# Kernel optimization log

Measured on AMD Instinct MI355X. Metric: run time of the kernel, lower is better.

## Reference

```python
import jax, jax.numpy as jnp
import numpy as np

K = 2          # diffusion steps
HID = 64       # hidden_dim
T_OUT = 12     # decoder horizon
EPS = 1e-6


def _random_walk(A):
    # W_fwd = D_out^{-1} A ; W_bwd = D_in^{-1} A^T  (row-normalized)
    W_fwd = A / (A.sum(axis=1, keepdims=True) + EPS)
    AT = A.T
    W_bwd = AT / (AT.sum(axis=1, keepdims=True) + EPS)
    return W_fwd, W_bwd


def _dconv(xin, Wf, Wb, W, b):
    # xin: (B, N, F). K forward + K backward random-walk hops, concat, linear.
    outs = [xin]
    xf = xin
    for _ in range(K):
        xf = jnp.einsum('ij,bjf->bif', Wf, xf)
        outs.append(xf)
    xb = xin
    for _ in range(K):
        xb = jnp.einsum('ij,bjf->bif', Wb, xb)
        outs.append(xb)
    return jnp.concatenate(outs, axis=-1) @ W + b


def _cell(xl, h, Wr, br, Wz, bz, Wn, bn, Wf, Wb):
    xh = jnp.concatenate([xl, h], axis=-1)
    r = jax.nn.sigmoid(_dconv(xh, Wf, Wb, Wr, br))
    z = jax.nn.sigmoid(_dconv(xh, Wf, Wb, Wz, bz))
    xrh = jnp.concatenate([xl, r * h], axis=-1)
    n = jnp.tanh(_dconv(xrh, Wf, Wb, Wn, bn))
    return (1.0 - z) * h + z * n


def setup_inputs() -> dict:
    key = jax.random.key(0)
    ks = jax.random.split(key, 20)
    B, T_in, N = 16, 12, 512
    x = jax.random.normal(ks[0], (B, T_in, N), dtype=jnp.float32)
    A = jax.random.uniform(ks[1], (N, N), dtype=jnp.float32)

    def lin(k, fan_in, fan_out):
        s = 1.0 / np.sqrt(fan_in)
        kw, kb = jax.random.split(k)
        W = jax.random.uniform(kw, (fan_in, fan_out), jnp.float32, -s, s)
        b = jax.random.uniform(kb, (fan_out,), jnp.float32, -s, s)
        return W, b

    in0 = (2 * K + 1) * (1 + HID)    # 325
    in1 = (2 * K + 1) * (2 * HID)    # 640
    Wr0, br0 = lin(ks[2], in0, HID)
    Wz0, bz0 = lin(ks[3], in0, HID)
    Wn0, bn0 = lin(ks[4], in0, HID)
    Wr1, br1 = lin(ks[5], in1, HID)
    Wz1, bz1 = lin(ks[6], in1, HID)
    Wn1, bn1 = lin(ks[7], in1, HID)
    Wp, bp = lin(ks[8], HID, 1)
    return dict(x=x, A=A, Wr0=Wr0, br0=br0, Wz0=Wz0, bz0=bz0, Wn0=Wn0, bn0=bn0,
                Wr1=Wr1, br1=br1, Wz1=Wz1, bz1=bz1, Wn1=Wn1, bn1=bn1, Wp=Wp, bp=bp)


def reference(x, A, Wr0, br0, Wz0, bz0, Wn0, bn0,
              Wr1, br1, Wz1, bz1, Wn1, bn1, Wp, bp):
    Wf, Wb = _random_walk(A)
    B, T_in, N = x.shape
    x4 = x[..., None]                             # (B, T_in, N, 1)
    h0 = jnp.zeros((B, N, HID), x.dtype)
    h1 = jnp.zeros((B, N, HID), x.dtype)

    def enc_step(carry, xt):
        h0, h1 = carry
        h0 = _cell(xt, h0, Wr0, br0, Wz0, bz0, Wn0, bn0, Wf, Wb)
        h1 = _cell(h0, h1, Wr1, br1, Wz1, bz1, Wn1, bn1, Wf, Wb)
        return (h0, h1), None

    (h0, h1), _ = jax.lax.scan(enc_step, (h0, h1), jnp.moveaxis(x4, 1, 0))

    def dec_step(carry, _):
        h0, h1, di = carry
        h0 = _cell(di, h0, Wr0, br0, Wz0, bz0, Wn0, bn0, Wf, Wb)
        h1 = _cell(h0, h1, Wr1, br1, Wz1, bz1, Wn1, bn1, Wf, Wb)
        yt = h1 @ Wp + bp                          # (B, N, 1)
        return (h0, h1, yt), yt

    (_, _, _), ys = jax.lax.scan(dec_step, (h0, h1, x4[:, -1]), None, length=T_OUT)
    return jnp.moveaxis(ys, 0, 1)[..., 0]          # (B, T_out, N)
```

## Files before the change

### kernel.cpp

```cpp
#include <hip/hip_runtime.h>
#include <math.h>

#define T_IN   12
#define T_OUT  12
#define NB     8192
#define EPSV   1e-6f

typedef __attribute__((ext_vector_type(8))) short short8;
typedef __attribute__((ext_vector_type(4))) float floatx4;

__device__ __forceinline__ unsigned short f2bf(float x) {
    union { float f; unsigned u; } v; v.f = x;
    unsigned r = v.u + 0x7fffu + ((v.u >> 16) & 1u);
    return (unsigned short)(r >> 16);
}
__device__ __forceinline__ float bf2f(unsigned short h) {
    union { float f; unsigned u; } v; v.u = ((unsigned)h) << 16;
    return v.f;
}
__device__ __forceinline__ unsigned packbf(float v) {
    unsigned u = __float_as_uint(v);
    unsigned hu = u & 0xffff0000u;
    float r = v - __uint_as_float(hu);
    unsigned ru = __float_as_uint(r);
    return (ru & 0xffff0000u) | (u >> 16);
}

__device__ __forceinline__ float sigmoid_fast(float x) {
    return 1.0f / (1.0f + __expf(-x));
}
__device__ __forceinline__ float tanh_fast(float x) {
    float e = __expf(2.0f * x);
    return 1.0f - 2.0f / (e + 1.0f);
}

struct HopA {
    const float* M[4];
    float* dst0[4];
};

struct HopM {
    const unsigned short* Ahi[4]; const unsigned short* Alo[4];
    const unsigned* src0; const unsigned* src1;
    unsigned* dst0[4]; unsigned* dst1[4];
    int tiles0;
};

struct XHopAll { const float* M[4]; const float* xenc; float* dst; };
struct XHopOne { const float* M[4]; const float* xv; float* dst; };

struct WPack { const float* w[4]; unsigned short* hi[4]; unsigned short* lo[4]; };

struct LPack {
    const float* W; unsigned short* hi; unsigned short* lo;
    int base[10]; int nseg;
};

struct LinA {
    const unsigned* seg[10]; int nseg;
    const float* sx[5]; int sxrow[5]; int nsx;
};

__global__ void sums_kernel(const float* __restrict__ A, float* __restrict__ rs,
                            float* __restrict__ cs) {
    int i = blockIdx.x;
    int t = threadIdx.x;
    __shared__ float s1[256], s2[256];
    float a = A[i * 512 + t] + A[i * 512 + t + 256];
    float b = A[t * 512 + i] + A[(t + 256) * 512 + i];
    s1[t] = a; s2[t] = b;
    __syncthreads();
    for (int off = 128; off > 0; off >>= 1) {
        if (t < off) { s1[t] += s1[t + off]; s2[t] += s2[t + off]; }
        __syncthreads();
    }
    if (t == 0) { rs[i] = s1[0]; cs[i] = s2[0]; }
}

__global__ void fill_kernel(const float* __restrict__ A, const float* __restrict__ rs,
                            const float* __restrict__ cs, float* __restrict__ Wf,
                            float* __restrict__ Wb) {
    int i = blockIdx.x;
    float irs = 1.0f / (rs[i] + EPSV);
    float ics = 1.0f / (cs[i] + EPSV);
    for (int j = threadIdx.x; j < 512; j += 256) {
        Wf[i * 512 + j] = A[i * 512 + j] * irs;
        Wb[i * 512 + j] = A[j * 512 + i] * ics;
    }
}

__global__ void xenc_kernel(const float* __restrict__ x, float* __restrict__ xenc) {
    int idx = blockIdx.x * 256 + threadIdx.x;
    if (idx >= T_IN * NB) return;
    int j = idx & 511;
    int b = (idx >> 9) & 15;
    int t = idx >> 13;
    xenc[t * NB + j * 16 + b] = x[(b * T_IN + t) * 512 + j];
}

__global__ __launch_bounds__(256) void ghop_kernel(HopA a) {
    int z = blockIdx.z;
    const float* Wm = a.M[z];
    const float* X = Wm;
    float* Y = a.dst0[z];
    int col0 = blockIdx.x * 64;
    int row0 = blockIdx.y * 64;
    int tid = threadIdx.x;
    int tx = tid & 15, ty = tid >> 4;
    int kkA = tid & 15, rrA = tid >> 4;
    int ccB = tid & 63, kkB = tid >> 6;

    __shared__ float As[16][68], Bs[16][68];
    float acc[4][4] = {};

    const float* wp = Wm + (row0 + rrA) * 512 + kkA;
    const float* xp = X + (size_t)(col0 + ccB) + (size_t)kkB * 512;

    float ra[4], rb[4];
#pragma unroll
    for (int p = 0; p < 4; ++p) ra[p] = wp[p * 16 * 512];
#pragma unroll
    for (int p = 0; p < 4; ++p) rb[p] = xp[(size_t)(p * 4) * 512];

    for (int k0 = 0; k0 < 512; k0 += 16) {
#pragma unroll
        for (int p = 0; p < 4; ++p) As[kkA][rrA + p * 16] = ra[p];
#pragma unroll
        for (int p = 0; p < 4; ++p) Bs[kkB + p * 4][ccB] = rb[p];
        __syncthreads();
        if (k0 + 16 < 512) {
            int kn = k0 + 16;
#pragma unroll
            for (int p = 0; p < 4; ++p) ra[p] = wp[p * 16 * 512 + kn];
#pragma unroll
            for (int p = 0; p < 4; ++p) rb[p] = xp[(size_t)(kn + p * 4) * 512];
        }
#pragma unroll
        for (int k = 0; k < 16; ++k) {
            const float4 a4 = *(const float4*)&As[k][ty * 4];
            const float4 b4 = *(const float4*)&Bs[k][tx * 4];
            float av[4] = { a4.x, a4.y, a4.z, a4.w };
            float bv[4] = { b4.x, b4.y, b4.z, b4.w };
#pragma unroll
            for (int i = 0; i < 4; ++i)
#pragma unroll
                for (int j = 0; j < 4; ++j)
                    acc[i][j] = fmaf(av[i], bv[j], acc[i][j]);
        }
        __syncthreads();
    }

    int colw = col0 + tx * 4;
#pragma unroll
    for (int i = 0; i < 4; ++i) {
        int row = row0 + ty * 4 + i;
        *(float4*)&Y[(size_t)row * 512 + colw] =
            make_float4(acc[i][0], acc[i][1], acc[i][2], acc[i][3]);
    }
}

__global__ void wpack_kernel(WPack a) {
    int z = blockIdx.y;
    int idx = blockIdx.x * 256 + threadIdx.x;
    int m = idx >> 9, k = idx & 511;
    float x = a.w[z][idx];
    unsigned short h = f2bf(x);
    unsigned short l = f2bf(x - bf2f(h));
    int p = (((m >> 4) * 64 + (k >> 3)) * 16 + (m & 15)) * 8 + (k & 7);
    a.hi[z][p] = h;
    a.lo[z][p] = l;
}

__global__ void lpack_kernel(LPack p) {
    int idx = blockIdx.x * 256 + threadIdx.x;
    if (idx >= p.nseg * 4096) return;
    int j = idx & 7, ln = (idx >> 3) & 15, ntl = (idx >> 7) & 3, O = idx >> 9;
    int s = O >> 3, o8 = O & 7;
    int row = p.base[s] + o8 * 8 + j;
    int col = ntl * 16 + ln;
    float v = p.W[(size_t)row * 64 + col];
    unsigned short h = f2bf(v);
    p.hi[idx] = h;
    p.lo[idx] = f2bf(v - bf2f(h));
}

__global__ void xhop_all_kernel(XHopAll a) {
    int t = blockIdx.z, mz = blockIdx.y;
    int m = blockIdx.x * 16 + (threadIdx.x >> 4);
    int c = threadIdx.x & 15;
    const float* wrow = a.M[mz] + (size_t)m * 512;
    const float* xv = a.xenc + (size_t)t * NB;
    float s[8] = {};
    for (int k = 0; k < 512; k += 8) {
        float4 w0 = *(const float4*)&wrow[k];
        float4 w1 = *(const float4*)&wrow[k + 4];
        s[0] = fmaf(w0.x, xv[(k + 0) * 16 + c], s[0]);
        s[1] = fmaf(w0.y, xv[(k + 1) * 16 + c], s[1]);
        s[2] = fmaf(w0.z, xv[(k + 2) * 16 + c], s[2]);
        s[3] = fmaf(w0.w, xv[(k + 3) * 16 + c], s[3]);
        s[4] = fmaf(w1.x, xv[(k + 4) * 16 + c], s[4]);
        s[5] = fmaf(w1.y, xv[(k + 5) * 16 + c], s[5]);
        s[6] = fmaf(w1.z, xv[(k + 6) * 16 + c], s[6]);
        s[7] = fmaf(w1.w, xv[(k + 7) * 16 + c], s[7]);
    }
    float r = ((s[0] + s[1]) + (s[2] + s[3])) + ((s[4] + s[5]) + (s[6] + s[7]));
    a.dst[((size_t)t * 4 + mz) * NB + m * 16 + c] = r;
}

__global__ void xhop_one_kernel(XHopOne a) {
    int mz = blockIdx.y;
    int m = blockIdx.x * 16 + (threadIdx.x >> 4);
    int c = threadIdx.x & 15;
    const float* wrow = a.M[mz] + (size_t)m * 512;
    const float* xv = a.xv;
    float s[8] = {};
    for (int k = 0; k < 512; k += 8) {
        float4 w0 = *(const float4*)&wrow[k];
        float4 w1 = *(const float4*)&wrow[k + 4];
        s[0] = fmaf(w0.x, xv[(k + 0) * 16 + c], s[0]);
        s[1] = fmaf(w0.y, xv[(k + 1) * 16 + c], s[1]);
        s[2] = fmaf(w0.z, xv[(k + 2) * 16 + c], s[2]);
        s[3] = fmaf(w0.w, xv[(k + 3) * 16 + c], s[3]);
        s[4] = fmaf(w1.x, xv[(k + 4) * 16 + c], s[4]);
        s[5] = fmaf(w1.y, xv[(k + 5) * 16 + c], s[5]);
        s[6] = fmaf(w1.z, xv[(k + 6) * 16 + c], s[6]);
        s[7] = fmaf(w1.w, xv[(k + 7) * 16 + c], s[7]);
    }
    float r = ((s[0] + s[1]) + (s[2] + s[3])) + ((s[4] + s[5]) + (s[6] + s[7]));
    a.dst[(size_t)mz * NB + m * 16 + c] = r;
}

template<int MI>
__global__ __launch_bounds__(256) void hop_mfma(HopM a) {
    int z = blockIdx.z;
    int nt = blockIdx.x;
    const unsigned* X; unsigned* Y; int c0;
    if (nt < a.tiles0) { X = a.src0; Y = a.dst0[z]; c0 = nt * 64; }
    else { X = a.src1; Y = a.dst1[z]; c0 = (nt - a.tiles0) * 64; }
    const unsigned short* Ahi = a.Ahi[z];
    const unsigned short* Alo = a.Alo[z];
    int bm = blockIdx.y * (MI * 32);

    __shared__ unsigned short Bhi_s[2][64][40];
    __shared__ unsigned short Blo_s[2][64][40];

    int tid = threadIdx.x;
    int lane = tid & 63, w = tid >> 6;
    int wm = (w & 1) * (MI * 16), wn = (w >> 1) * 32;
    int ln = lane & 15, quad = lane >> 4;
    int sc = tid & 63, skh = tid >> 6;

    floatx4 acc[MI][2];
#pragma unroll
    for (int mi = 0; mi < MI; ++mi)
#pragma unroll
        for (int ci = 0; ci < 2; ++ci) acc[mi][ci] = (floatx4)0.0f;

    const unsigned* xbase = X + c0 + sc;
    int mtb = (bm + wm) >> 4;

    unsigned uv[8];
#pragma unroll
    for (int j = 0; j < 8; ++j)
        uv[j] = xbase[(size_t)(skh * 8 + j) * 1024];
    {
        short8 h8, l8;
#pragma unroll
        for (int j = 0; j < 8; ++j) {
            h8[j] = (short)(uv[j] & 0xffffu);
            l8[j] = (short)(uv[j] >> 16);
        }
        *(short8*)&Bhi_s[0][sc][skh * 8] = h8;
        *(short8*)&Blo_s[0][sc][skh * 8] = l8;
    }
#pragma unroll
    for (int j = 0; j < 8; ++j)
        uv[j] = xbase[(size_t)(32 + skh * 8 + j) * 1024];

    for (int it = 0; it < 16; ++it) {
        __syncthreads();
        int cur = it & 1;
        if (it + 1 < 16) {
            short8 h8, l8;
#pragma unroll
            for (int j = 0; j < 8; ++j) {
                h8[j] = (short)(uv[j] & 0xffffu);
                l8[j] = (short)(uv[j] >> 16);
            }
            *(short8*)&Bhi_s[cur ^ 1][sc][skh * 8] = h8;
            *(short8*)&Blo_s[cur ^ 1][sc][skh * 8] = l8;
        }
        if (it + 2 < 16) {
            int kn = (it + 2) * 32;
#pragma unroll
            for (int j = 0; j < 8; ++j)
                uv[j] = xbase[(size_t)(kn + skh * 8 + j) * 1024];
        }
        short8 bh[2], bl[2];
#pragma unroll
        for (int ci = 0; ci < 2; ++ci) {
            bh[ci] = *(const short8*)&Bhi_s[cur][wn + ci * 16 + ln][quad * 8];
            bl[ci] = *(const short8*)&Blo_s[cur][wn + ci * 16 + ln][quad * 8];
        }
        int kob = it * 4 + quad;
#pragma unroll
        for (int mi = 0; mi < MI; ++mi) {
            size_t aoff = ((size_t)((mtb + mi) * 64 + kob) * 16 + ln) * 8;
            short8 Ah = *(const short8*)(Ahi + aoff);
            short8 Al = *(const short8*)(Alo + aoff);
#pragma unroll
            for (int ci = 0; ci < 2; ++ci) {
                acc[mi][ci] = __builtin_amdgcn_mfma_f32_16x16x32_bf16(Ah, bh[ci], acc[mi][ci], 0, 0, 0);
                acc[mi][ci] = __builtin_amdgcn_mfma_f32_16x16x32_bf16(Ah, bl[ci], acc[mi][ci], 0, 0, 0);
                acc[mi][ci] = __builtin_amdgcn_mfma_f32_16x16x32_bf16(Al, bh[ci], acc[mi][ci], 0, 0, 0);
            }
        }
    }

#pragma unroll
    for (int mi = 0; mi < MI; ++mi) {
#pragma unroll
        for (int ci = 0; ci < 2; ++ci) {
            int mrow = bm + wm + mi * 16 + quad * 4;
            int col = c0 + wn + ci * 16 + ln;
#pragma unroll
            for (int r = 0; r < 4; ++r)
                Y[(size_t)(mrow + r) * 1024 + col] = packbf(acc[mi][ci][r]);
        }
    }
}

__device__ __forceinline__ void lin_core2(const LinA& a,
        const unsigned short* __restrict__ Bh, const unsigned short* __restrict__ Bl,
        int row0, int ln, int quad, int cihalf, floatx4 acc[2]) {
    for (int s = 0; s < a.nseg; ++s) {
        const unsigned* ap = a.seg[s] + (size_t)(row0 + ln) * 64 + quad * 8;
#pragma unroll
        for (int hh = 0; hh < 2; ++hh) {
            unsigned u[8];
            *(uint4*)&u[0] = *(const uint4*)(ap + hh * 32);
            *(uint4*)&u[4] = *(const uint4*)(ap + hh * 32 + 4);
            short8 Ah, Al;
#pragma unroll
            for (int j = 0; j < 8; ++j) {
                Ah[j] = (short)(u[j] & 0xffffu);
                Al[j] = (short)(u[j] >> 16);
            }
            int O = s * 8 + hh * 4 + quad;
#pragma unroll
            for (int ci = 0; ci < 2; ++ci) {
                int c_abs = cihalf * 2 + ci;
                size_t boff = ((size_t)(O * 4 + c_abs) * 16 + ln) * 8;
                short8 B1 = *(const short8*)(Bh + boff);
                short8 B2 = *(const short8*)(Bl + boff);
                acc[ci] = __builtin_amdgcn_mfma_f32_16x16x32_bf16(Ah, B1, acc[ci], 0, 0, 0);
                acc[ci] = __builtin_amdgcn_mfma_f32_16x16x32_bf16(Al, B1, acc[ci], 0, 0, 0);
                acc[ci] = __builtin_amdgcn_mfma_f32_16x16x32_bf16(Ah, B2, acc[ci], 0, 0, 0);
            }
        }
    }
}

__device__ __forceinline__ void lin_scalar2(const LinA& a, const float* __restrict__ WO,
        int row0, int ln, int quad, int cihalf, floatx4 acc[2]) {
    for (int t = 0; t < a.nsx; ++t) {
        const float* wr = WO + (size_t)a.sxrow[t] * 64;
        const float* sv = a.sx[t] + row0 + quad * 4;
#pragma unroll
        for (int rr = 0; rr < 4; ++rr) {
            float v = sv[rr];
#pragma unroll
            for (int ci = 0; ci < 2; ++ci)
                acc[ci][rr] = fmaf(v, wr[(cihalf * 2 + ci) * 16 + ln], acc[ci][rr]);
        }
    }
}

__global__ __launch_bounds__(256) void lin_rz_mfma(
    LinA a,
    const unsigned short* Wrh, const unsigned short* Wrl, const float* WrO, const float* br,
    const unsigned short* Wzh, const unsigned short* Wzl, const float* WzO, const float* bz,
    const float* __restrict__ h, unsigned* __restrict__ GP, float* __restrict__ Z) {
    int w = threadIdx.x >> 6, lane = threadIdx.x & 63;
    int ln = lane & 15, quad = lane >> 4;
    int row0 = blockIdx.x * 64 + w * 16;
    int gate = blockIdx.y;
    int cihalf = blockIdx.z;
    const unsigned short* Bh = gate ? Wzh : Wrh;
    const unsigned short* Bl = gate ? Wzl : Wrl;
    const float* WO = gate ? WzO : WrO;
    const float* bias = gate ? bz : br;
    floatx4 acc[2];
    acc[0] = (floatx4)0.0f; acc[1] = (floatx4)0.0f;
    lin_core2(a, Bh, Bl, row0, ln, quad, cihalf, acc);
    if (a.nsx) lin_scalar2(a, WO, row0, ln, quad, cihalf, acc);
#pragma unroll
    for (int ci = 0; ci < 2; ++ci) {
        int col = (cihalf * 2 + ci) * 16 + ln;
        float bv = bias[col];
#pragma unroll
        for (int rr = 0; rr < 4; ++rr) {
            int row = row0 + quad * 4 + rr;
            size_t idx = (size_t)row * 64 + col;
            float sg = sigmoid_fast(acc[ci][rr] + bv);
            if (gate == 0) GP[idx] = packbf(sg * h[idx]);
            else Z[idx] = sg;
        }
    }
}

__global__ __launch_bounds__(256) void lin_n_mfma(
    LinA a, const unsigned short* Wnh, const unsigned short* Wnl,
    const float* WnO, const float* bn,
    const float* __restrict__ Zb, float* __restrict__ h, unsigned* __restrict__ hP,
    int doProj, const float* __restrict__ Wp, const float* __restrict__ bp,
    float* __restrict__ out, float* __restrict__ di, int t) {
    int w = threadIdx.x >> 6, lane = threadIdx.x & 63;
    int ln = lane & 15, quad = lane >> 4;
    int cihalf = w & 1, rsub = w >> 1;
    int row0 = (blockIdx.x * 2 + rsub) * 16;
    __shared__ float pr[2][2][16];
    floatx4 acc[2];
    acc[0] = (floatx4)0.0f; acc[1] = (floatx4)0.0f;
    lin_core2(a, Wnh, Wnl, row0, ln, quad, cihalf, acc);
    if (a.nsx) lin_scalar2(a, WnO, row0, ln, quad, cihalf, acc);
    float p[4] = {0.0f, 0.0f, 0.0f, 0.0f};
#pragma unroll
    for (int ci = 0; ci < 2; ++ci) {
        int col = (cihalf * 2 + ci) * 16 + ln;
        float bv = bn[col];
        float wpv = doProj ? Wp[col] : 0.0f;
#pragma unroll
        for (int rr = 0; rr < 4; ++rr) {
            int row = row0 + quad * 4 + rr;
            size_t idx = (size_t)row * 64 + col;
            float nn = tanh_fast(acc[ci][rr] + bv);
            float z = Zb[idx];
            float hv = h[idx];
            float o = (1.0f - z) * hv + z * nn;
            h[idx] = o;
            hP[idx] = packbf(o);
            p[rr] = fmaf(o, wpv, p[rr]);
        }
    }
    if (doProj) {
#pragma unroll
        for (int rr = 0; rr < 4; ++rr) {
            p[rr] += __shfl_xor(p[rr], 1, 64);
            p[rr] += __shfl_xor(p[rr], 2, 64);
            p[rr] += __shfl_xor(p[rr], 4, 64);
            p[rr] += __shfl_xor(p[rr], 8, 64);
        }
        if (ln == 0) {
#pragma unroll
            for (int rr = 0; rr < 4; ++rr)
                pr[cihalf][rsub][quad * 4 + rr] = p[rr];
        }
        __syncthreads();
        if (cihalf == 0 && ln == 0) {
            float bpv = bp[0];
#pragma unroll
            for (int rr = 0; rr < 4; ++rr) {
                int qr = quad * 4 + rr;
                int row = row0 + qr;
                float y = pr[0][rsub][qr] + pr[1][rsub][qr] + bpv;
                int n = row >> 4, b = row & 15;
                out[(b * T_OUT + t) * 512 + n] = y;
                di[row] = y;
            }
        }
    }
}

extern "C" void kernel_launch(void* const* d_in, const int* in_sizes, int n_in,
                              void* d_out, int out_size, void* d_ws, size_t ws_size,
                              hipStream_t stream) {
    (void)in_sizes; (void)n_in; (void)out_size; (void)ws_size;
    const float* x   = (const float*)d_in[0];
    const float* A   = (const float*)d_in[1];
    const float* Wr0 = (const float*)d_in[2];  const float* br0 = (const float*)d_in[3];
    const float* Wz0 = (const float*)d_in[4];  const float* bz0 = (const float*)d_in[5];
    const float* Wn0 = (const float*)d_in[6];  const float* bn0 = (const float*)d_in[7];
    const float* Wr1 = (const float*)d_in[8];  const float* br1 = (const float*)d_in[9];
    const float* Wz1 = (const float*)d_in[10]; const float* bz1 = (const float*)d_in[11];
    const float* Wn1 = (const float*)d_in[12]; const float* bn1 = (const float*)d_in[13];
    const float* Wp  = (const float*)d_in[14]; const float* bp  = (const float*)d_in[15];
    float* out = (float*)d_out;

    float* ws = (float*)d_ws;
    size_t off = 0;
    auto alloc = [&](size_t nf) { float* p = ws + off; off += nf; return p; };
    float* Wf  = alloc(262144); float* Wb  = alloc(262144);
    float* W2f = alloc(262144); float* W2b = alloc(262144);
    float* rs  = alloc(512);    float* cs  = alloc(512);
    float* xenc = alloc((size_t)T_IN * NB);
    unsigned short* Whi[4]; unsigned short* Wlo[4];
    for (int m = 0; m < 4; ++m) Whi[m] = (unsigned short*)alloc(131072);
    for (int m = 0; m < 4; ++m) Wlo[m] = (unsigned short*)alloc(131072);
    unsigned* HAall = (unsigned*)alloc(4 * 524288);
    unsigned* HA_P[4]; for (int m = 0; m < 4; ++m) HA_P[m] = HAall + (size_t)m * 524288;
    unsigned* HB_P[4]; unsigned* HG_P[4];
    for (int m = 0; m < 4; ++m) HB_P[m] = (unsigned*)alloc(524288);
    for (int m = 0; m < 4; ++m) HG_P[m] = (unsigned*)alloc(524288);
    unsigned* GP  = (unsigned*)alloc(524288);
    unsigned* h0P = (unsigned*)alloc(524288);
    unsigned* h1P = (unsigned*)alloc(524288);
    float* Z  = alloc(524288);
    float* h0 = alloc(524288);
    float* h1 = alloc(524288);
    float* XHE = alloc((size_t)T_IN * 4 * NB);
    float* HXSdec = alloc(4 * NB);
    float* di = alloc(NB);
    unsigned short* LWh[6]; unsigned short* LWl[6];
    for (int g = 0; g < 3; ++g) { LWh[g] = (unsigned short*)alloc(10240); LWl[g] = (unsigned short*)alloc(10240); }
    for (int g = 3; g < 6; ++g) { LWh[g] = (unsigned short*)alloc(20480); LWl[g] = (unsigned short*)alloc(20480); }

    hipMemsetAsync(h0, 0, 524288 * sizeof(float), stream);
    hipMemsetAsync(h1, 0, 524288 * sizeof(float), stream);
    hipMemsetAsync(h0P, 0, 524288 * sizeof(unsigned), stream);
    hipMemsetAsync(h1P, 0, 524288 * sizeof(unsigned), stream);
    hipMemsetAsync(HAall, 0, 4ul * 524288 * sizeof(unsigned), stream);

    xenc_kernel<<<dim3((T_IN * NB) / 256), 256, 0, stream>>>(x, xenc);
    sums_kernel<<<dim3(512), 256, 0, stream>>>(A, rs, cs);
    fill_kernel<<<dim3(512), 256, 0, stream>>>(A, rs, cs, Wf, Wb);

    {
        HopA w2 = {};
        w2.M[0] = Wf; w2.M[1] = Wb;
        w2.dst0[0] = W2f; w2.dst0[1] = W2b;
        ghop_kernel<<<dim3(8, 8, 2), 256, 0, stream>>>(w2);
    }
    {
        WPack p;
        p.w[0] = Wf; p.w[1] = W2f; p.w[2] = Wb; p.w[3] = W2b;
        for (int m = 0; m < 4; ++m) { p.hi[m] = Whi[m]; p.lo[m] = Wlo[m]; }
        wpack_kernel<<<dim3(1024, 4), 256, 0, stream>>>(p);
    }
    {
        const float* WG[6] = { Wr0, Wz0, Wn0, Wr1, Wz1, Wn1 };
        for (int g = 0; g < 6; ++g) {
            LPack p = {};
            p.W = WG[g]; p.hi = LWh[g]; p.lo = LWl[g];
            if (g < 3) { p.nseg = 5;  for (int s = 0; s < 5; ++s)  p.base[s] = 65 * s + 1; }
            else       { p.nseg = 10; for (int s = 0; s < 10; ++s) p.base[s] = 64 * s; }
            lpack_kernel<<<dim3((p.nseg * 4096 + 255) / 256), 256, 0, stream>>>(p);
        }
    }
    {
        XHopAll xa;
        xa.M[0] = Wf; xa.M[1] = W2f; xa.M[2] = Wb; xa.M[3] = W2b;
        xa.xenc = xenc; xa.dst = XHE;
        xhop_all_kernel<<<dim3(32, 4, T_IN), 256, 0, stream>>>(xa);
    }

    auto hopcom = [&](HopM& a) {
        for (int m = 0; m < 4; ++m) { a.Ahi[m] = Whi[m]; a.Alo[m] = Wlo[m]; }
    };

    for (int t = 0; t < T_IN + T_OUT; ++t) {
        int dec = (t >= T_IN);
        int td = t - T_IN;
        const float* xcur; const float* hxs;
        if (!dec) { xcur = xenc + (size_t)t * NB; hxs = XHE + (size_t)t * 4 * NB; }
        else if (td == 0) { xcur = xenc + (size_t)(T_IN - 1) * NB; hxs = XHE + (size_t)(T_IN - 1) * 4 * NB; }
        else {
            xcur = di; hxs = HXSdec;
            XHopOne xo;
            xo.M[0] = Wf; xo.M[1] = W2f; xo.M[2] = Wb; xo.M[3] = W2b;
            xo.xv = di; xo.dst = HXSdec;
            xhop_one_kernel<<<dim3(32, 4), 256, 0, stream>>>(xo);
        }

        LinA la = {};
        la.nseg = 5;
        la.seg[0] = h0P;
        for (int m = 0; m < 4; ++m) la.seg[1 + m] = HA_P[m];
        la.nsx = 5;
        la.sx[0] = xcur; la.sxrow[0] = 0;
        for (int m = 0; m < 4; ++m) { la.sx[1 + m] = hxs + (size_t)m * NB; la.sxrow[1 + m] = 65 * (m + 1); }
        lin_rz_mfma<<<dim3(128, 2, 2), 256, 0, stream>>>(la, LWh[0], LWl[0], Wr0, br0,
                                                         LWh[1], LWl[1], Wz0, bz0, h0, GP, Z);
        {
            HopM a = {}; hopcom(a);
            a.src0 = GP; a.tiles0 = 16;
            for (int m = 0; m < 4; ++m) a.dst0[m] = HG_P[m];
            hop_mfma<2><<<dim3(16, 8, 4), 256, 0, stream>>>(a);
        }
        LinA lb = la;
        lb.seg[0] = GP;
        for (int m = 0; m < 4; ++m) lb.seg[1 + m] = HG_P[m];
        lin_n_mfma<<<dim3(256), 256, 0, stream>>>(lb, LWh[2], LWl[2], Wn0, bn0, Z, h0, h0P,
                                                  0, (const float*)nullptr, (const float*)nullptr,
                                                  (float*)nullptr, (float*)nullptr, 0);

        {
            HopM a = {}; hopcom(a);
            a.src0 = h0P; a.tiles0 = 16;
            a.src1 = h1P;
            for (int m = 0; m < 4; ++m) { a.dst0[m] = HA_P[m]; a.dst1[m] = HB_P[m]; }
            hop_mfma<4><<<dim3(32, 4, 4), 256, 0, stream>>>(a);
        }
        LinA lc = {};
        lc.nseg = 10; lc.nsx = 0;
        lc.seg[0] = h0P; lc.seg[1] = h1P;
        for (int m = 0; m < 4; ++m) { lc.seg[2 + 2 * m] = HA_P[m]; lc.seg[3 + 2 * m] = HB_P[m]; }
        lin_rz_mfma<<<dim3(128, 2, 2), 256, 0, stream>>>(lc, LWh[3], LWl[3], Wr1, br1,
                                                         LWh[4], LWl[4], Wz1, bz1, h1, GP, Z);
        {
            HopM a = {}; hopcom(a);
            a.src0 = GP; a.tiles0 = 16;
            for (int m = 0; m < 4; ++m) a.dst0[m] = HG_P[m];
            hop_mfma<2><<<dim3(16, 8, 4), 256, 0, stream>>>(a);
        }
        LinA ld = lc;
        ld.seg[1] = GP;
        for (int m = 0; m < 4; ++m) ld.seg[3 + 2 * m] = HG_P[m];
        lin_n_mfma<<<dim3(256), 256, 0, stream>>>(ld, LWh[5], LWl[5], Wn1, bn1, Z, h1, h1P,
                                                  dec, Wp, bp, out, di, td);
    }
}
```

Baseline: 3.246 ms.

## Use MFMA for input diffusion hops, split-K lin_n, and smaller hop tiles

Measured after the change: 2.963 ms. -8.7%, faster.

```diff
diff --git a/kernel.cpp b/kernel.cpp
--- a/kernel.cpp
+++ b/kernel.cpp
@@ -25,6 +25,12 @@
     unsigned ru = __float_as_uint(r);
     return (ru & 0xffff0000u) | (u >> 16);
 }
+__device__ __forceinline__ void split2(float v, short& h, short& l) {
+    unsigned u = __float_as_uint(v);
+    h = (short)(u >> 16);
+    float r = v - __uint_as_float(u & 0xffff0000u);
+    l = (short)(__float_as_uint(r) >> 16);
+}
 
 __device__ __forceinline__ float sigmoid_fast(float x) {
     return 1.0f / (1.0f + __expf(-x));
@@ -46,8 +52,12 @@
     int tiles0;
 };
 
-struct XHopAll { const float* M[4]; const float* xenc; float* dst; };
-struct XHopOne { const float* M[4]; const float* xv; float* dst; };
+struct XHopM {
+    const unsigned short* Ahi[4]; const unsigned short* Alo[4];
+    const float* X;
+    float* Y;
+    int ncols;
+};
 
 struct WPack { const float* w[4]; unsigned short* hi[4]; unsigned short* lo[4]; };
 
@@ -184,52 +194,6 @@
     p.lo[idx] = f2bf(v - bf2f(h));
 }
 
-__global__ void xhop_all_kernel(XHopAll a) {
-    int t = blockIdx.z, mz = blockIdx.y;
-    int m = blockIdx.x * 16 + (threadIdx.x >> 4);
-    int c = threadIdx.x & 15;
-    const float* wrow = a.M[mz] + (size_t)m * 512;
-    const float* xv = a.xenc + (size_t)t * NB;
-    float s[8] = {};
-    for (int k = 0; k < 512; k += 8) {
-        float4 w0 = *(const float4*)&wrow[k];
-        float4 w1 = *(const float4*)&wrow[k + 4];
-        s[0] = fmaf(w0.x, xv[(k + 0) * 16 + c], s[0]);
-        s[1] = fmaf(w0.y, xv[(k + 1) * 16 + c], s[1]);
-        s[2] = fmaf(w0.z, xv[(k + 2) * 16 + c], s[2]);
-        s[3] = fmaf(w0.w, xv[(k + 3) * 16 + c], s[3]);
-        s[4] = fmaf(w1.x, xv[(k + 4) * 16 + c], s[4]);
-        s[5] = fmaf(w1.y, xv[(k + 5) * 16 + c], s[5]);
-        s[6] = fmaf(w1.z, xv[(k + 6) * 16 + c], s[6]);
-        s[7] = fmaf(w1.w, xv[(k + 7) * 16 + c], s[7]);
-    }
-    float r = ((s[0] + s[1]) + (s[2] + s[3])) + ((s[4] + s[5]) + (s[6] + s[7]));
-    a.dst[((size_t)t * 4 + mz) * NB + m * 16 + c] = r;
-}
-
-__global__ void xhop_one_kernel(XHopOne a) {
-    int mz = blockIdx.y;
-    int m = blockIdx.x * 16 + (threadIdx.x >> 4);
-    int c = threadIdx.x & 15;
-    const float* wrow = a.M[mz] + (size_t)m * 512;
-    const float* xv = a.xv;
-    float s[8] = {};
-    for (int k = 0; k < 512; k += 8) {
-        float4 w0 = *(const float4*)&wrow[k];
-        float4 w1 = *(const float4*)&wrow[k + 4];
-        s[0] = fmaf(w0.x, xv[(k + 0) * 16 + c], s[0]);
-        s[1] = fmaf(w0.y, xv[(k + 1) * 16 + c], s[1]);
-        s[2] = fmaf(w0.z, xv[(k + 2) * 16 + c], s[2]);
-        s[3] = fmaf(w0.w, xv[(k + 3) * 16 + c], s[3]);
-        s[4] = fmaf(w1.x, xv[(k + 4) * 16 + c], s[4]);
-        s[5] = fmaf(w1.y, xv[(k + 5) * 16 + c], s[5]);
-        s[6] = fmaf(w1.z, xv[(k + 6) * 16 + c], s[6]);
-        s[7] = fmaf(w1.w, xv[(k + 7) * 16 + c], s[7]);
-    }
-    float r = ((s[0] + s[1]) + (s[2] + s[3])) + ((s[4] + s[5]) + (s[6] + s[7]));
-    a.dst[(size_t)mz * NB + m * 16 + c] = r;
-}
-
 template<int MI>
 __global__ __launch_bounds__(256) void hop_mfma(HopM a) {
     int z = blockIdx.z;
@@ -330,11 +294,106 @@
     }
 }
 
-__device__ __forceinline__ void lin_core2(const LinA& a,
+__global__ __launch_bounds__(256) void xhop_mfma(XHopM a) {
+    int z = blockIdx.z;
+    int c0 = blockIdx.x * 64;
+    const unsigned short* Ahi = a.Ahi[z];
+    const unsigned short* Alo = a.Alo[z];
+    int bm = blockIdx.y * 64;
+
+    __shared__ unsigned short Bhi_s[2][64][40];
+    __shared__ unsigned short Blo_s[2][64][40];
+
+    int tid = threadIdx.x;
+    int lane = tid & 63, w = tid >> 6;
+    int wm = (w & 1) * 32, wn = (w >> 1) * 32;
+    int ln = lane & 15, quad = lane >> 4;
+    int sc = tid & 63, skh = tid >> 6;
+
+    floatx4 acc[2][2];
+#pragma unroll
+    for (int mi = 0; mi < 2; ++mi)
+#pragma unroll
+        for (int ci = 0; ci < 2; ++ci) acc[mi][ci] = (floatx4)0.0f;
+
+    int colS = c0 + sc;
+    bool ok = colS < a.ncols;
+    const float* xb = a.X + (size_t)(colS >> 4) * NB + (colS & 15);
+    int mtb = (bm + wm) >> 4;
+
+    float xv[8];
+#pragma unroll
+    for (int j = 0; j < 8; ++j)
+        xv[j] = ok ? xb[(size_t)(skh * 8 + j) * 16] : 0.0f;
+    {
+        short8 h8, l8;
+#pragma unroll
+        for (int j = 0; j < 8; ++j) { short h, l; split2(xv[j], h, l); h8[j] = h; l8[j] = l; }
+        *(short8*)&Bhi_s[0][sc][skh * 8] = h8;
+        *(short8*)&Blo_s[0][sc][skh * 8] = l8;
+    }
+#pragma unroll
+    for (int j = 0; j < 8; ++j)
+        xv[j] = ok ? xb[(size_t)(32 + skh * 8 + j) * 16] : 0.0f;
+
+    for (int it = 0; it < 16; ++it) {
+        __syncthreads();
+        int cur = it & 1;
+        if (it + 1 < 16) {
+            short8 h8, l8;
+#pragma unroll
+            for (int j = 0; j < 8; ++j) { short h, l; split2(xv[j], h, l); h8[j] = h; l8[j] = l; }
+            *(short8*)&Bhi_s[cur ^ 1][sc][skh * 8] = h8;
+            *(short8*)&Blo_s[cur ^ 1][sc][skh * 8] = l8;
+        }
+        if (it + 2 < 16) {
+            int kn = (it + 2) * 32;
+#pragma unroll
+            for (int j = 0; j < 8; ++j)
+                xv[j] = ok ? xb[(size_t)(kn + skh * 8 + j) * 16] : 0.0f;
+        }
+        short8 bh[2], bl[2];
+#pragma unroll
+        for (int ci = 0; ci < 2; ++ci) {
+            bh[ci] = *(const short8*)&Bhi_s[cur][wn + ci * 16 + ln][quad * 8];
+            bl[ci] = *(const short8*)&Blo_s[cur][wn + ci * 16 + ln][quad * 8];
+        }
+        int kob = it * 4 + quad;
+#pragma unroll
+        for (int mi = 0; mi < 2; ++mi) {
+            size_t aoff = ((size_t)((mtb + mi) * 64 + kob) * 16 + ln) * 8;
+            short8 Ah = *(const short8*)(Ahi + aoff);
+            short8 Al = *(const short8*)(Alo + aoff);
+#pragma unroll
+            for (int ci = 0; ci < 2; ++ci) {
+                acc[mi][ci] = __builtin_amdgcn_mfma_f32_16x16x32_bf16(Ah, bh[ci], acc[mi][ci], 0, 0, 0);
+                acc[mi][ci] = __builtin_amdgcn_mfma_f32_16x16x32_bf16(Ah, bl[ci], acc[mi][ci], 0, 0, 0);
+                acc[mi][ci] = __builtin_amdgcn_mfma_f32_16x16x32_bf16(Al, bh[ci], acc[mi][ci], 0, 0, 0);
+            }
+        }
+    }
+
+#pragma unroll
+    for (int mi = 0; mi < 2; ++mi) {
+#pragma unroll
+        for (int ci = 0; ci < 2; ++ci) {
+            int col = c0 + wn + ci * 16 + ln;
+            if (col < a.ncols) {
+                int mrow = bm + wm + mi * 16 + quad * 4;
+                float* yb = a.Y + (size_t)((col >> 4) * 4 + z) * NB + (col & 15);
+#pragma unroll
+                for (int r = 0; r < 4; ++r)
+                    yb[(size_t)(mrow + r) * 16] = acc[mi][ci][r];
+            }
+        }
+    }
+}
+
+__device__ __forceinline__ void lin_core2(const unsigned* const* segs, int nseg, int s0,
         const unsigned short* __restrict__ Bh, const unsigned short* __restrict__ Bl,
         int row0, int ln, int quad, int cihalf, floatx4 acc[2]) {
-    for (int s = 0; s < a.nseg; ++s) {
-        const unsigned* ap = a.seg[s] + (size_t)(row0 + ln) * 64 + quad * 8;
+    for (int s = 0; s < nseg; ++s) {
+        const unsigned* ap = segs[s] + (size_t)(row0 + ln) * 64 + quad * 8;
 #pragma unroll
         for (int hh = 0; hh < 2; ++hh) {
             unsigned u[8];
@@ -346,7 +405,7 @@
                 Ah[j] = (short)(u[j] & 0xffffu);
                 Al[j] = (short)(u[j] >> 16);
             }
-            int O = s * 8 + hh * 4 + quad;
+            int O = (s0 + s) * 8 + hh * 4 + quad;
 #pragma unroll
             for (int ci = 0; ci < 2; ++ci) {
                 int c_abs = cihalf * 2 + ci;
@@ -392,7 +451,7 @@
     const float* bias = gate ? bz : br;
     floatx4 acc[2];
     acc[0] = (floatx4)0.0f; acc[1] = (floatx4)0.0f;
-    lin_core2(a, Bh, Bl, row0, ln, quad, cihalf, acc);
+    lin_core2(a.seg, a.nseg, 0, Bh, Bl, row0, ln, quad, cihalf, acc);
     if (a.nsx) lin_scalar2(a, WO, row0, ln, quad, cihalf, acc);
 #pragma unroll
     for (int ci = 0; ci < 2; ++ci) {
@@ -410,64 +469,79 @@
 }
 
 __global__ __launch_bounds__(256) void lin_n_mfma(
-    LinA a, const unsigned short* Wnh, const unsigned short* Wnl,
+    LinA a, int ksplit,
+    const unsigned short* Wnh, const unsigned short* Wnl,
     const float* WnO, const float* bn,
     const float* __restrict__ Zb, float* __restrict__ h, unsigned* __restrict__ hP,
     int doProj, const float* __restrict__ Wp, const float* __restrict__ bp,
     float* __restrict__ out, float* __restrict__ di, int t) {
     int w = threadIdx.x >> 6, lane = threadIdx.x & 63;
     int ln = lane & 15, quad = lane >> 4;
-    int cihalf = w & 1, rsub = w >> 1;
-    int row0 = (blockIdx.x * 2 + rsub) * 16;
-    __shared__ float pr[2][2][16];
+    int kh = w & 1, cihalf = w >> 1;
+    int row0 = blockIdx.x * 16;
+    __shared__ float part[2][2][16][17];
+    __shared__ float pr[2][16];
     floatx4 acc[2];
     acc[0] = (floatx4)0.0f; acc[1] = (floatx4)0.0f;
-    lin_core2(a, Wnh, Wnl, row0, ln, quad, cihalf, acc);
-    if (a.nsx) lin_scalar2(a, WnO, row0, ln, quad, cihalf, acc);
+    if (kh == 0) {
+        lin_core2(a.seg, ksplit, 0, Wnh, Wnl, row0, ln, quad, cihalf, acc);
+    } else {
+        lin_core2(a.seg + ksplit, a.nseg - ksplit, ksplit, Wnh, Wnl, row0, ln, quad, cihalf, acc);
+        if (a.nsx) lin_scalar2(a, WnO, row0, ln, quad, cihalf, acc);
+#pragma unroll
+        for (int ci = 0; ci < 2; ++ci)
+#pragma unroll
+            for (int rr = 0; rr < 4; ++rr)
+                part[cihalf][ci][quad * 4 + rr][ln] = acc[ci][rr];
+    }
+    __syncthreads();
     float p[4] = {0.0f, 0.0f, 0.0f, 0.0f};
-#pragma unroll
-    for (int ci = 0; ci < 2; ++ci) {
-        int col = (cihalf * 2 + ci) * 16 + ln;
-        float bv = bn[col];
-        float wpv = doProj ? Wp[col] : 0.0f;
+    if (kh == 0) {
+#pragma unroll
+        for (int ci = 0; ci < 2; ++ci) {
+            int col = (cihalf * 2 + ci) * 16 + ln;
+            float bv = bn[col];
+            float wpv = doProj ? Wp[col] : 0.0f;
+#pragma unroll
+            for (int rr = 0; rr < 4; ++rr) {
+                int row = row0 + quad * 4 + rr;
+                size_t idx = (size_t)row * 64 + col;
+                float pre = acc[ci][rr] + part[cihalf][ci][quad * 4 + rr][ln] + bv;
+                float nn = tanh_fast(pre);
+                float z = Zb[idx];
+                float hv = h[idx];
+                float o = (1.0f - z) * hv + z * nn;
+                h[idx] = o;
+                hP[idx] = packbf(o);
+                p[rr] = fmaf(o, wpv, p[rr]);
+            }
+        }
+        if (doProj) {
+#pragma unroll
+            for (int rr = 0; rr < 4; ++rr) {
+                p[rr] += __shfl_xor(p[rr], 1, 64);
+                p[rr] += __shfl_xor(p[rr], 2, 64);
+                p[rr] += __shfl_xor(p[rr], 4, 64);
+                p[rr] += __shfl_xor(p[rr], 8, 64);
+            }
+            if (ln == 0) {
+#pragma unroll
+                for (int rr = 0; rr < 4; ++rr)
+                    pr[cihalf][quad * 4 + rr] = p[rr];
+            }
+        }
+    }
+    __syncthreads();
+    if (doProj && kh == 0 && cihalf == 0 && ln == 0) {
+        float bpv = bp[0];
 #pragma unroll
         for (int rr = 0; rr < 4; ++rr) {
-            int row = row0 + quad * 4 + rr;
-            size_t idx = (size_t)row * 64 + col;
-            float nn = tanh_fast(acc[ci][rr] + bv);
-            float z = Zb[idx];
-            float hv = h[idx];
-            float o = (1.0f - z) * hv + z * nn;
-            h[idx] = o;
-            hP[idx] = packbf(o);
-            p[rr] = fmaf(o, wpv, p[rr]);
-        }
-    }
-    if (doProj) {
-#pragma unroll
-        for (int rr = 0; rr < 4; ++rr) {
-            p[rr] += __shfl_xor(p[rr], 1, 64);
-            p[rr] += __shfl_xor(p[rr], 2, 64);
-            p[rr] += __shfl_xor(p[rr], 4, 64);
-            p[rr] += __shfl_xor(p[rr], 8, 64);
-        }
-        if (ln == 0) {
-#pragma unroll
-            for (int rr = 0; rr < 4; ++rr)
-                pr[cihalf][rsub][quad * 4 + rr] = p[rr];
-        }
-        __syncthreads();
-        if (cihalf == 0 && ln == 0) {
-            float bpv = bp[0];
-#pragma unroll
-            for (int rr = 0; rr < 4; ++rr) {
-                int qr = quad * 4 + rr;
-                int row = row0 + qr;
-                float y = pr[0][rsub][qr] + pr[1][rsub][qr] + bpv;
-                int n = row >> 4, b = row & 15;
-                out[(b * T_OUT + t) * 512 + n] = y;
-                di[row] = y;
-            }
+            int qr = quad * 4 + rr;
+            int row = row0 + qr;
+            float y = pr[0][qr] + pr[1][qr] + bpv;
+            int n = row >> 4, b = row & 15;
+            out[(b * T_OUT + t) * 512 + n] = y;
+            di[row] = y;
         }
     }
 }
@@ -548,10 +622,10 @@
         }
     }
     {
-        XHopAll xa;
-        xa.M[0] = Wf; xa.M[1] = W2f; xa.M[2] = Wb; xa.M[3] = W2b;
-        xa.xenc = xenc; xa.dst = XHE;
-        xhop_all_kernel<<<dim3(32, 4, T_IN), 256, 0, stream>>>(xa);
+        XHopM xa = {};
+        for (int m = 0; m < 4; ++m) { xa.Ahi[m] = Whi[m]; xa.Alo[m] = Wlo[m]; }
+        xa.X = xenc; xa.Y = XHE; xa.ncols = 192;
+        xhop_mfma<<<dim3(3, 8, 4), 256, 0, stream>>>(xa);
     }
 
     auto hopcom = [&](HopM& a) {
@@ -566,10 +640,10 @@
         else if (td == 0) { xcur = xenc + (size_t)(T_IN - 1) * NB; hxs = XHE + (size_t)(T_IN - 1) * 4 * NB; }
         else {
             xcur = di; hxs = HXSdec;
-            XHopOne xo;
-            xo.M[0] = Wf; xo.M[1] = W2f; xo.M[2] = Wb; xo.M[3] = W2b;
-            xo.xv = di; xo.dst = HXSdec;
-            xhop_one_kernel<<<dim3(32, 4), 256, 0, stream>>>(xo);
+            XHopM xo = {};
+            for (int m = 0; m < 4; ++m) { xo.Ahi[m] = Whi[m]; xo.Alo[m] = Wlo[m]; }
+            xo.X = di; xo.Y = HXSdec; xo.ncols = 16;
+            xhop_mfma<<<dim3(1, 8, 4), 256, 0, stream>>>(xo);
         }
 
         LinA la = {};
@@ -585,12 +659,12 @@
             HopM a = {}; hopcom(a);
             a.src0 = GP; a.tiles0 = 16;
             for (int m = 0; m < 4; ++m) a.dst0[m] = HG_P[m];
-            hop_mfma<2><<<dim3(16, 8, 4), 256, 0, stream>>>(a);
+            hop_mfma<1><<<dim3(16, 16, 4), 256, 0, stream>>>(a);
         }
         LinA lb = la;
         lb.seg[0] = GP;
         for (int m = 0; m < 4; ++m) lb.seg[1 + m] = HG_P[m];
-        lin_n_mfma<<<dim3(256), 256, 0, stream>>>(lb, LWh[2], LWl[2], Wn0, bn0, Z, h0, h0P,
+        lin_n_mfma<<<dim3(512), 256, 0, stream>>>(lb, 3, LWh[2], LWl[2], Wn0, bn0, Z, h0, h0P,
                                                   0, (const float*)nullptr, (const float*)nullptr,
                                                   (float*)nullptr, (float*)nullptr, 0);
 
@@ -599,7 +673,7 @@
             a.src0 = h0P; a.tiles0 = 16;
             a.src1 = h1P;
             for (int m = 0; m < 4; ++m) { a.dst0[m] = HA_P[m]; a.dst1[m] = HB_P[m]; }
-            hop_mfma<4><<<dim3(32, 4, 4), 256, 0, stream>>>(a);
+            hop_mfma<2><<<dim3(32, 8, 4), 256, 0, stream>>>(a);
         }
         LinA lc = {};
         lc.nseg = 10; lc.nsx = 0;
@@ -611,12 +685,12 @@
             HopM a = {}; hopcom(a);
             a.src0 = GP; a.tiles0 = 16;
             for (int m = 0; m < 4; ++m) a.dst0[m] = HG_P[m];
-            hop_mfma<2><<<dim3(16, 8, 4), 256, 0, stream>>>(a);
+            hop_mfma<1><<<dim3(16, 16, 4), 256, 0, stream>>>(a);
         }
         LinA ld = lc;
         ld.seg[1] = GP;
         for (int m = 0; m < 4; ++m) ld.seg[3 + 2 * m] = HG_P[m];
-        lin_n_mfma<<<dim3(256), 256, 0, stream>>>(ld, LWh[5], LWl[5], Wn1, bn1, Z, h1, h1P,
+        lin_n_mfma<<<dim3(512), 256, 0, stream>>>(ld, 5, LWh[5], LWl[5], Wn1, bn1, Z, h1, h1P,
                                                   dec, Wp, bp, out, di, td);
     }
 }
```
